# Performance work log

Hardware: AMD Instinct MI355X
Metric: run time of the kernel (lower is better)

## Reference

```python
import jax, jax.numpy as jnp
import numpy as np


def setup_inputs() -> dict:
    key = jax.random.key(0)
    ks = jax.random.split(key, 12)
    B, L, N, C, Ct, H, RH1, RH2, S = 64, 64, 256, 8, 4, 128, 128, 64, 4
    def rn(k, shape, s=0.08):
        return jax.random.normal(k, shape, dtype=jnp.float32) * s
    return dict(
        x=jax.random.normal(ks[0], (B, L, N, C * Ct), dtype=jnp.float32),
        hidden_intensity=jax.random.normal(ks[1], (B, N, H), dtype=jnp.float32),
        r=jax.random.normal(ks[2], (B, S), dtype=jnp.float32),
        W_ih=rn(ks[3], (4 * H, C)), W_hh=rn(ks[4], (4 * H, H)),
        b_ih=jnp.zeros((4 * H,), jnp.float32), b_hh=jnp.zeros((4 * H,), jnp.float32),
        W1=rn(ks[5], (RH1, 2 * H + 1)), b1=jnp.zeros((RH1,), jnp.float32),
        W2=rn(ks[6], (RH2, RH1)), b2=jnp.zeros((RH2,), jnp.float32),
        W3=rn(ks[7], (C, RH2)), b3=jnp.zeros((C,), jnp.float32),
        Wf=rn(ks[8], (1, C)), bf=jnp.zeros((1,), jnp.float32),
    )


def reference(x, hidden_intensity, r, W_ih, W_hh, b_ih, b_hh,
              W1, b1, W2, b2, W3, b3, Wf, bf):
    # Faithful to torch: nn.LSTM has batch_first=False but is fed (B, L, C),
    # so B is the sequence axis, L the batch axis, and lstm_out[:, -1, :]
    # writes predictions into that last column, so only x[:, -1] matters.
    B, L, N, _ = x.shape
    C = W_ih.shape[1]
    Ct = x.shape[3] // C
    H = W_hh.shape[1]

    def lstm_all_times(seq):  # seq: (T, Bb, C) -> hidden at every time (T, Bb, H)
        xp = jnp.einsum('tbc,gc->tbg', seq, W_ih) + b_ih + b_hh  # (T, Bb, 4H)
        def step(carry, xt):
            h, c = carry
            g = xt + h @ W_hh.T
            i, f, gg, o = jnp.split(g, 4, axis=-1)  # torch gate order i,f,g,o
            c = jax.nn.sigmoid(f) * c + jax.nn.sigmoid(i) * jnp.tanh(gg)
            h = jax.nn.sigmoid(o) * jnp.tanh(c)
            return (h, c), h
        z0 = jnp.zeros((seq.shape[1], H), seq.dtype)
        _, hs = jax.lax.scan(step, (z0, z0), xp)
        return hs

    hi = jnp.broadcast_to(hidden_intensity[:, :, None, :], (B, N, Ct, H))

    def roll(last_col, rj):  # last_col: (B, N, Ct, C), rj: (B,)
        hs = lstm_all_times(last_col.reshape(B, N * Ct, C)).reshape(B, N, Ct, H)
        rr = jnp.broadcast_to(rj[:, None, None, None], (B, N, Ct, 1))
        z = jnp.concatenate([hs, hi, rr], axis=-1)       # (B, N, Ct, 2H+1)
        h1 = jax.nn.relu(z @ W1.T + b1)
        h2 = jax.nn.relu(h1 @ W2.T + b2)
        pr = h2 @ W3.T + b3                              # (B, N, Ct, C)
        contrib = (jax.nn.relu(pr) @ Wf.T + bf)[..., 0].sum(axis=2)  # (B, N)
        return pr, contrib

    last0 = x[:, -1, :, :].reshape(B, N, Ct, C)
    _, preds = jax.lax.scan(roll, last0, r.T)  # (S, B, N)
    return jnp.transpose(preds, (1, 2, 0))     # (B, N, steps_ahead)
```

## Files before the change

### kernel.cpp

```cpp
#include <hip/hip_runtime.h>
#include <hip/hip_bf16.h>


typedef __attribute__((ext_vector_type(8))) _Float16 half8;
typedef __attribute__((ext_vector_type(4))) float f32x4;

#define MFMAH(a, b, c) __builtin_amdgcn_mfma_f32_16x16x32_f16(a, b, c, 0, 0, 0)

__device__ __forceinline__ float sigf(float x)   { return 1.0f / (1.0f + __expf(-x)); }
__device__ __forceinline__ float tanh_f(float x) { return 1.0f - 2.0f / (__expf(2.0f * x) + 1.0f); }

__global__ void prep_k(const float* __restrict__ x, const float* __restrict__ hi,
                       const float* __restrict__ W1, const float* __restrict__ W2,
                       const float* __restrict__ W3, const float* __restrict__ W_hh,
                       const float* __restrict__ W_ih,
                       _Float16* __restrict__ cur16, _Float16* __restrict__ hi16,
                       _Float16* __restrict__ wp1, _Float16* __restrict__ wp2,
                       _Float16* __restrict__ wp3, _Float16* __restrict__ wpB)
{
    int i = blockIdx.x * 256 + threadIdx.x;
    if (i < 65536) {
        int e = i * 8;
        int b = e >> 13, rem = e & 8191;
        const float* src = x + (size_t)b * 524288 + 63 * 8192 + rem;
        half8 v;
#pragma unroll
        for (int k = 0; k < 8; ++k) v[k] = (_Float16)src[k];
        *(half8*)(cur16 + e) = v;
        return;
    }
    i -= 65536;
    if (i < 262144) {
        int e = i * 8;
        half8 v;
#pragma unroll
        for (int k = 0; k < 8; ++k) v[k] = (_Float16)hi[e + k];
        *(half8*)(hi16 + e) = v;
        return;
    }
    i -= 262144;
    if (i < 32768) {
        int fragid = i >> 9, lj = i & 511;
        int kt = fragid >> 3, nt = fragid & 7;
        int l = lj >> 3, j = lj & 7;
        int k = kt * 32 + (l >> 4) * 8 + j;
        int o = nt * 16 + (l & 15);
        wp1[i] = (_Float16)W1[o * 257 + k];
        return;
    }
    i -= 32768;
    if (i < 8192) {
        int fragid = i >> 9, lj = i & 511;
        int kt = fragid >> 2, nt = fragid & 3;
        int l = lj >> 3, j = lj & 7;
        int k = kt * 32 + (l >> 4) * 8 + j;
        int o = nt * 16 + (l & 15);
        wp2[i] = (_Float16)W2[o * 128 + k];
        return;
    }
    i -= 8192;
    if (i < 1024) {
        int kt = i >> 9, lj = i & 511;
        int l = lj >> 3, j = lj & 7;
        int k = kt * 32 + (l >> 4) * 8 + j;
        int c = l & 15;
        wp3[i] = (_Float16)((c < 8) ? W3[c * 64 + k] : 0.0f);
        return;
    }
    i -= 1024;
    if (i < 81920) {
        int frag = i >> 9, lj = i & 511;
        int kt = frag >> 5, ntile = frag & 31;
        int l = lj >> 3, j = lj & 7;
        int klocal = (l >> 4) * 8 + j;
        int col = ntile * 16 + (l & 15);
        float v;
        if (kt < 4) v = W_hh[col * 128 + kt * 32 + klocal];
        else        v = (klocal < 8) ? W_ih[col * 8 + klocal] : 0.0f;
        wpB[i] = (_Float16)v;
    }
}

__global__ __launch_bounds__(512, 2) void lstm_mfma_k(
    const _Float16* __restrict__ cur16, const _Float16* __restrict__ wpB,
    const float* __restrict__ b_ih, const float* __restrict__ b_hh,
    _Float16* __restrict__ hs16)
{
    __shared__ __align__(16) _Float16 zone[2][4][640];
    __shared__ __align__(16) _Float16 xz[64][32];

    const int t  = threadIdx.x;
    const int cg = t >> 6, l = t & 63;
    const int li = l & 15, lk = l >> 4;
    const int q0 = blockIdx.x * 4;

    const int gsrc[4] = {1, 0, 2, 3};
    half8 bw[4][5];
#pragma unroll
    for (int g = 0; g < 4; ++g)
#pragma unroll
        for (int kt = 0; kt < 5; ++kt) {
            bw[g][kt] = *(const half8*)(wpB + (size_t)(kt * 32 + gsrc[g] * 8 + cg) * 512 + l * 8);
            asm volatile("" : "+a"(bw[g][kt]));
        }

    f32x4 bs4[4];
#pragma unroll
    for (int g = 0; g < 4; ++g) {
        int gc = gsrc[g] * 128 + cg * 16 + li;
        float bv = b_ih[gc] + b_hh[gc];
        bs4[g] = (f32x4){bv, bv, bv, bv};
    }

    for (int i = t; i < 1280; i += 512) ((uint*)zone)[i] = 0;
    if (t < 256) {
        int step = t >> 2, tt = t & 3;
        *(uint4*)&xz[step][tt * 8] =
            *(const uint4*)(cur16 + (size_t)step * 8192 + q0 * 8 + tt * 8);
    }
    float cc = 0.0f;
    __syncthreads();

    const int zpl   = cg >> 1;
    const int jl    = (cg & 1) * 16 + li;
    const int roff  = (li & 12) * 40 + lk * 8;
    const int srow  = lk * 4;

    _Float16* ph = hs16 + (size_t)(q0 + lk) * 128 + cg * 16 + li;
    const _Float16* xrd = &xz[0][(li >> 2) * 8];

    f32x4 accx[4];
    {
        half8 xa0 = *(const half8*)(xrd);
#pragma unroll
        for (int g = 0; g < 4; ++g)
            accx[g] = MFMAH(xa0, bw[g][4], bs4[g]);
    }

    auto dostep = [&](int step, int p) {
        const int pn = p ^ 1;

        half8 ah[4];
#pragma unroll
        for (int kt = 0; kt < 4; ++kt)
            ah[kt] = *(const half8*)&zone[p][kt][roff];

        __builtin_amdgcn_s_setprio(1);
        const f32x4 z4 = (f32x4){0.0f, 0.0f, 0.0f, 0.0f};
        f32x4 a0[4], a1[4];
#pragma unroll
        for (int g = 0; g < 4; ++g) {
            a0[g] = MFMAH(ah[0], bw[g][0], accx[g]);
            a1[g] = MFMAH(ah[2], bw[g][2], z4);
        }
#pragma unroll
        for (int g = 0; g < 4; ++g) {
            a0[g] = MFMAH(ah[1], bw[g][1], a0[g]);
            a1[g] = MFMAH(ah[3], bw[g][3], a1[g]);
        }

        float pf = a0[0][0] + a1[0][0];
        float sf = sigf(pf);
        float pi = a0[1][0] + a1[1][0];
        float pg = a0[2][0] + a1[2][0];
        float po = a0[3][0] + a1[3][0];
        cc = sf * cc + sigf(pi) * tanh_f(pg);
        float hv = sigf(po) * tanh_f(cc);
        __builtin_amdgcn_s_setprio(0);
        _Float16 h16 = (_Float16)hv;
        zone[pn][zpl][srow * 40 + jl] = h16;
        ph[(size_t)step * 131072] = h16;
        asm volatile("s_waitcnt lgkmcnt(0)\n\ts_barrier" ::: "memory");

        half8 xn = *(const half8*)(xrd + ((step + 1) & 63) * 32);
#pragma unroll
        for (int g = 0; g < 4; ++g)
            accx[g] = MFMAH(xn, bw[g][4], bs4[g]);
    };

    for (int s2 = 0; s2 < 32; ++s2) {
        dostep(s2 * 2,     0);
        dostep(s2 * 2 + 1, 1);
    }
}

__global__ __launch_bounds__(256, 3) void mlp_mfma_k(
    const _Float16* __restrict__ hs16, const _Float16* __restrict__ hi16,
    const float* __restrict__ r, int jstep,
    const _Float16* __restrict__ wp1, const _Float16* __restrict__ wp2,
    const _Float16* __restrict__ wp3,
    const float* __restrict__ W1, const float* __restrict__ b1,
    const float* __restrict__ b2, const float* __restrict__ b3,
    const float* __restrict__ Wf, const float* __restrict__ bfp,
    _Float16* __restrict__ cur16, float* __restrict__ out)
{
    __shared__ __align__(16) _Float16 h1f[4 * 4 * 640];
    __shared__ __align__(16) _Float16 h2f[2 * 4 * 640];

    const int t = threadIdx.x;
    const int w = t >> 6, l = t & 63;
    const int lrow = l & 15, lk = l >> 4;
    const int b = blockIdx.x >> 4;
    const int qb = (blockIdx.x & 15) * 64;
    const float rb = r[b * 4 + jstep];

    f32x4 acc[4][2];
#pragma unroll
    for (int nt = 0; nt < 2; ++nt) {
        int col = w * 32 + nt * 16 + lrow;
        float bias = b1[col] + rb * W1[col * 257 + 256];
#pragma unroll
        for (int mt = 0; mt < 4; ++mt)
            acc[mt][nt] = (f32x4){bias, bias, bias, bias};
    }

    auto loadA = [&](int kt, half8* av) {
#pragma unroll
        for (int mt = 0; mt < 4; ++mt) {
            int q = qb + mt * 16 + lrow;
            if (kt < 4)
                av[mt] = *(const half8*)(hs16 + (size_t)(b * 1024 + q) * 128
                                          + kt * 32 + lk * 8);
            else
                av[mt] = *(const half8*)(hi16 + (size_t)(b * 256 + (q >> 2)) * 128
                                          + (kt - 4) * 32 + lk * 8);
        }
    };

    half8 avA[4], avB[4];
    loadA(0, avA);
#pragma unroll
    for (int kt = 0; kt < 8; ++kt) {
        half8* cur = (kt & 1) ? avB : avA;
        half8* nxt = (kt & 1) ? avA : avB;
        if (kt < 7) loadA(kt + 1, nxt);
#pragma unroll
        for (int nt = 0; nt < 2; ++nt) {
            half8 bv = *(const half8*)(wp1 + (size_t)(kt * 8 + w * 2 + nt) * 512 + l * 8);
#pragma unroll
            for (int mt = 0; mt < 4; ++mt)
                acc[mt][nt] = MFMAH(cur[mt], bv, acc[mt][nt]);
        }
    }

#pragma unroll
    for (int mt = 0; mt < 4; ++mt)
#pragma unroll
        for (int nt = 0; nt < 2; ++nt)
#pragma unroll
            for (int reg = 0; reg < 4; ++reg) {
                float v = fmaxf(acc[mt][nt][reg], 0.0f);
                int s = lk * 4 + reg, jj = nt * 16 + lrow;
                h1f[(w * 4 + mt) * 640 + s * 40 + jj] = (_Float16)v;
            }
    __syncthreads();

    f32x4 acc2[4];
    {
        float bias = b2[16 * w + lrow];
#pragma unroll
        for (int mt = 0; mt < 4; ++mt)
            acc2[mt] = (f32x4){bias, bias, bias, bias};
    }
#pragma unroll
    for (int kt = 0; kt < 4; ++kt) {
        half8 bv = *(const half8*)(wp2 + (size_t)(kt * 4 + w) * 512 + l * 8);
#pragma unroll
        for (int mt = 0; mt < 4; ++mt) {
            half8 a = *(const half8*)&h1f[(kt * 4 + mt) * 640 + lrow * 40 + lk * 8];
            acc2[mt] = MFMAH(a, bv, acc2[mt]);
        }
    }
#pragma unroll
    for (int mt = 0; mt < 4; ++mt)
#pragma unroll
        for (int reg = 0; reg < 4; ++reg) {
            float v = fmaxf(acc2[mt][reg], 0.0f);
            int s = lk * 4 + reg, jl2 = (w & 1) * 16 + lrow;
            h2f[((w >> 1) * 4 + mt) * 640 + s * 40 + jl2] = (_Float16)v;
        }
    __syncthreads();

    f32x4 acc3 = (f32x4){0.0f, 0.0f, 0.0f, 0.0f};
#pragma unroll
    for (int kt = 0; kt < 2; ++kt) {
        half8 a  = *(const half8*)&h2f[(kt * 4 + w) * 640 + lrow * 40 + lk * 8];
        half8 bv = *(const half8*)(wp3 + (size_t)kt * 512 + l * 8);
        acc3 = MFMAH(a, bv, acc3);
    }

    const int c = lrow;
    const float b3v = (c < 8) ? b3[c] : 0.0f;
    const float wfv = (c < 8) ? Wf[c] : 0.0f;
    float fr[4];
#pragma unroll
    for (int reg = 0; reg < 4; ++reg) {
        float pr = acc3[reg] + b3v;
        if (c < 8) {
            int row = 16 * w + lk * 4 + reg;
            cur16[((size_t)(b * 1024 + qb + row)) * 8 + c] = (_Float16)pr;
        }
        fr[reg] = (c < 8) ? fmaxf(pr, 0.0f) * wfv : 0.0f;
    }
#pragma unroll
    for (int reg = 0; reg < 4; ++reg) {
        fr[reg] += __shfl_xor(fr[reg], 1);
        fr[reg] += __shfl_xor(fr[reg], 2);
        fr[reg] += __shfl_xor(fr[reg], 4);
    }
    if ((l & 15) == 0) {
        int n = (qb + 16 * w + lk * 4) >> 2;
        float v = fr[0] + fr[1] + fr[2] + fr[3] + 4.0f * bfp[0];
        out[(size_t)(b * 256 + n) * 4 + jstep] = v;
    }
}

extern "C" void kernel_launch(void* const* d_in, const int* in_sizes, int n_in,
                              void* d_out, int out_size, void* d_ws, size_t ws_size,
                              hipStream_t stream)
{
    const float* x   = (const float*)d_in[0];
    const float* hi  = (const float*)d_in[1];
    const float* r   = (const float*)d_in[2];
    const float* Wih = (const float*)d_in[3];
    const float* Whh = (const float*)d_in[4];
    const float* bih = (const float*)d_in[5];
    const float* bhh = (const float*)d_in[6];
    const float* W1  = (const float*)d_in[7];
    const float* b1  = (const float*)d_in[8];
    const float* W2  = (const float*)d_in[9];
    const float* b2  = (const float*)d_in[10];
    const float* W3  = (const float*)d_in[11];
    const float* b3  = (const float*)d_in[12];
    const float* Wf  = (const float*)d_in[13];
    const float* bf  = (const float*)d_in[14];
    float* out = (float*)d_out;

    _Float16* cur16 = (_Float16*)d_ws;
    _Float16* hs16  = cur16 + 524288;
    _Float16* hi16  = hs16 + 8388608;
    _Float16* wp1   = hi16 + 2097152;
    _Float16* wp2   = wp1 + 32768;
    _Float16* wp3   = wp2 + 8192;
    _Float16* wpB   = wp3 + 1024;

    prep_k<<<1764, 256, 0, stream>>>(x, hi, W1, W2, W3, Whh, Wih,
                                     cur16, hi16, wp1, wp2, wp3, wpB);
    for (int j = 0; j < 4; ++j) {
        lstm_mfma_k<<<256, 512, 0, stream>>>(cur16, wpB, bih, bhh, hs16);
        mlp_mfma_k<<<1024, 256, 0, stream>>>(hs16, hi16, r, j, wp1, wp2, wp3,
                                             W1, b1, b2, b3, Wf, bf, cur16, out);
    }
}
```

Measured before the change: 279.3 us.

## Split LSTM recurrence into 2-sequence blocks of 4 waves, 2 N-tiles per wave

```diff
diff --git a/kernel.cpp b/kernel.cpp
--- a/kernel.cpp
+++ b/kernel.cpp
@@ -81,101 +81,94 @@
     }
 }
 
-__global__ __launch_bounds__(512, 2) void lstm_mfma_k(
+__global__ __launch_bounds__(256, 2) void lstm_mfma_k(
     const _Float16* __restrict__ cur16, const _Float16* __restrict__ wpB,
     const float* __restrict__ b_ih, const float* __restrict__ b_hh,
     _Float16* __restrict__ hs16)
 {
-    __shared__ __align__(16) _Float16 zone[2][4][640];
-    __shared__ __align__(16) _Float16 xz[64][32];
+    __shared__ __align__(16) _Float16 zone[2][4][2][40];
+    __shared__ __align__(16) _Float16 xz[64][16];
 
     const int t  = threadIdx.x;
     const int cg = t >> 6, l = t & 63;
     const int li = l & 15, lk = l >> 4;
-    const int q0 = blockIdx.x * 4;
+    const int q0 = blockIdx.x * 2;
 
     const int gsrc[4] = {1, 0, 2, 3};
-    half8 bw[4][5];
+    half8 bw[4][2][5];
 #pragma unroll
     for (int g = 0; g < 4; ++g)
 #pragma unroll
-        for (int kt = 0; kt < 5; ++kt) {
-            bw[g][kt] = *(const half8*)(wpB + (size_t)(kt * 32 + gsrc[g] * 8 + cg) * 512 + l * 8);
-            asm volatile("" : "+a"(bw[g][kt]));
-        }
-
-    f32x4 bs4[4];
-#pragma unroll
-    for (int g = 0; g < 4; ++g) {
-        int gc = gsrc[g] * 128 + cg * 16 + li;
-        float bv = b_ih[gc] + b_hh[gc];
-        bs4[g] = (f32x4){bv, bv, bv, bv};
-    }
-
-    for (int i = t; i < 1280; i += 512) ((uint*)zone)[i] = 0;
-    if (t < 256) {
-        int step = t >> 2, tt = t & 3;
-        *(uint4*)&xz[step][tt * 8] =
-            *(const uint4*)(cur16 + (size_t)step * 8192 + q0 * 8 + tt * 8);
-    }
-    float cc = 0.0f;
+        for (int nt = 0; nt < 2; ++nt)
+#pragma unroll
+            for (int kt = 0; kt < 5; ++kt) {
+                bw[g][nt][kt] = *(const half8*)(wpB +
+                    (size_t)(kt * 32 + gsrc[g] * 8 + 2 * cg + nt) * 512 + l * 8);
+                asm volatile("" : "+a"(bw[g][nt][kt]));
+            }
+
+    float bias[4][2];
+#pragma unroll
+    for (int g = 0; g < 4; ++g)
+#pragma unroll
+        for (int nt = 0; nt < 2; ++nt) {
+            int gc = gsrc[g] * 128 + (2 * cg + nt) * 16 + li;
+            bias[g][nt] = b_ih[gc] + b_hh[gc];
+        }
+
+    if (t < 320) ((uint*)zone)[t] = 0;
+    if (t < 128) {
+        int step = t >> 1, s = t & 1;
+        *(uint4*)&xz[step][s * 8] =
+            *(const uint4*)(cur16 + (size_t)step * 8192 + (q0 + s) * 8);
+    }
+    float cc0 = 0.0f, cc1 = 0.0f;
     __syncthreads();
 
-    const int zpl   = cg >> 1;
-    const int jl    = (cg & 1) * 16 + li;
-    const int roff  = (li & 12) * 40 + lk * 8;
-    const int srow  = lk * 4;
-
-    _Float16* ph = hs16 + (size_t)(q0 + lk) * 128 + cg * 16 + li;
-    const _Float16* xrd = &xz[0][(li >> 2) * 8];
-
-    f32x4 accx[4];
-    {
-        half8 xa0 = *(const half8*)(xrd);
-#pragma unroll
-        for (int g = 0; g < 4; ++g)
-            accx[g] = MFMAH(xa0, bw[g][4], bs4[g]);
-    }
+    const int sli  = (li >> 2) & 1;
+    const int roff = sli * 40 + lk * 8;
+    const _Float16* xrd = &xz[0][sli * 8];
+
+    _Float16* ph = hs16 + (size_t)(q0 + lk) * 128 + cg * 32 + li;
+
+    const f32x4 z4 = (f32x4){0.0f, 0.0f, 0.0f, 0.0f};
 
     auto dostep = [&](int step, int p) {
         const int pn = p ^ 1;
-
+        half8 xa = *(const half8*)(xrd + step * 16);
         half8 ah[4];
 #pragma unroll
         for (int kt = 0; kt < 4; ++kt)
-            ah[kt] = *(const half8*)&zone[p][kt][roff];
+            ah[kt] = *(const half8*)&zone[p][kt][0][roff];
 
         __builtin_amdgcn_s_setprio(1);
-        const f32x4 z4 = (f32x4){0.0f, 0.0f, 0.0f, 0.0f};
-        f32x4 a0[4], a1[4];
+        float pv[4][2];
 #pragma unroll
         for (int g = 0; g < 4; ++g) {
-            a0[g] = MFMAH(ah[0], bw[g][0], accx[g]);
-            a1[g] = MFMAH(ah[2], bw[g][2], z4);
-        }
-#pragma unroll
-        for (int g = 0; g < 4; ++g) {
-            a0[g] = MFMAH(ah[1], bw[g][1], a0[g]);
-            a1[g] = MFMAH(ah[3], bw[g][3], a1[g]);
-        }
-
-        float pf = a0[0][0] + a1[0][0];
-        float sf = sigf(pf);
-        float pi = a0[1][0] + a1[1][0];
-        float pg = a0[2][0] + a1[2][0];
-        float po = a0[3][0] + a1[3][0];
-        cc = sf * cc + sigf(pi) * tanh_f(pg);
-        float hv = sigf(po) * tanh_f(cc);
+            f32x4 a0 = MFMAH(xa, bw[g][0][4], z4);
+            f32x4 a1 = MFMAH(xa, bw[g][1][4], z4);
+#pragma unroll
+            for (int kt = 0; kt < 4; ++kt) {
+                a0 = MFMAH(ah[kt], bw[g][0][kt], a0);
+                a1 = MFMAH(ah[kt], bw[g][1][kt], a1);
+            }
+            pv[g][0] = a0[0] + bias[g][0];
+            pv[g][1] = a1[0] + bias[g][1];
+        }
+
+        cc0 = sigf(pv[0][0]) * cc0 + sigf(pv[1][0]) * tanh_f(pv[2][0]);
+        float hv0 = sigf(pv[3][0]) * tanh_f(cc0);
+        cc1 = sigf(pv[0][1]) * cc1 + sigf(pv[1][1]) * tanh_f(pv[2][1]);
+        float hv1 = sigf(pv[3][1]) * tanh_f(cc1);
         __builtin_amdgcn_s_setprio(0);
-        _Float16 h16 = (_Float16)hv;
-        zone[pn][zpl][srow * 40 + jl] = h16;
-        ph[(size_t)step * 131072] = h16;
+        _Float16 h0 = (_Float16)hv0, h1 = (_Float16)hv1;
+        if (lk < 2) {
+            zone[pn][cg][lk][li]      = h0;
+            zone[pn][cg][lk][16 + li] = h1;
+            ph[(size_t)step * 131072]      = h0;
+            ph[(size_t)step * 131072 + 16] = h1;
+        }
         asm volatile("s_waitcnt lgkmcnt(0)\n\ts_barrier" ::: "memory");
-
-        half8 xn = *(const half8*)(xrd + ((step + 1) & 63) * 32);
-#pragma unroll
-        for (int g = 0; g < 4; ++g)
-            accx[g] = MFMAH(xn, bw[g][4], bs4[g]);
     };
 
     for (int s2 = 0; s2 < 32; ++s2) {
@@ -347,7 +340,7 @@
     prep_k<<<1764, 256, 0, stream>>>(x, hi, W1, W2, W3, Whh, Wih,
                                      cur16, hi16, wp1, wp2, wp3, wpB);
     for (int j = 0; j < 4; ++j) {
-        lstm_mfma_k<<<256, 512, 0, stream>>>(cur16, wpB, bih, bhh, hs16);
+        lstm_mfma_k<<<512, 256, 0, stream>>>(cur16, wpB, bih, bhh, hs16);
         mlp_mfma_k<<<1024, 256, 0, stream>>>(hs16, hi16, r, j, wp1, wp2, wp3,
                                              W1, b1, b2, b3, Wf, bf, cur16, out);
     }
```

Result: slower. 396.7 us (+42.0%).

## Fuse LSTM and MLP across all rollout steps into one persistent kernel

Applied to the files above, without the earlier changes.

```diff
diff --git a/kernel.cpp b/kernel.cpp
--- a/kernel.cpp
+++ b/kernel.cpp
@@ -10,26 +10,15 @@
 __device__ __forceinline__ float sigf(float x)   { return 1.0f / (1.0f + __expf(-x)); }
 __device__ __forceinline__ float tanh_f(float x) { return 1.0f - 2.0f / (__expf(2.0f * x) + 1.0f); }
 
-__global__ void prep_k(const float* __restrict__ x, const float* __restrict__ hi,
+__global__ void prep_k(const float* __restrict__ hi,
                        const float* __restrict__ W1, const float* __restrict__ W2,
                        const float* __restrict__ W3, const float* __restrict__ W_hh,
                        const float* __restrict__ W_ih,
-                       _Float16* __restrict__ cur16, _Float16* __restrict__ hi16,
-                       _Float16* __restrict__ wp1, _Float16* __restrict__ wp2,
-                       _Float16* __restrict__ wp3, _Float16* __restrict__ wpB)
+                       _Float16* __restrict__ hi16, _Float16* __restrict__ wp1,
+                       _Float16* __restrict__ wp2, _Float16* __restrict__ wp3,
+                       _Float16* __restrict__ wpB)
 {
     int i = blockIdx.x * 256 + threadIdx.x;
-    if (i < 65536) {
-        int e = i * 8;
-        int b = e >> 13, rem = e & 8191;
-        const float* src = x + (size_t)b * 524288 + 63 * 8192 + rem;
-        half8 v;
-#pragma unroll
-        for (int k = 0; k < 8; ++k) v[k] = (_Float16)src[k];
-        *(half8*)(cur16 + e) = v;
-        return;
-    }
-    i -= 65536;
     if (i < 262144) {
         int e = i * 8;
         half8 v;
@@ -39,16 +28,19 @@
         return;
     }
     i -= 262144;
-    if (i < 32768) {
+    if (i < 36864) {
         int fragid = i >> 9, lj = i & 511;
         int kt = fragid >> 3, nt = fragid & 7;
         int l = lj >> 3, j = lj & 7;
-        int k = kt * 32 + (l >> 4) * 8 + j;
+        int klocal = (l >> 4) * 8 + j;
         int o = nt * 16 + (l & 15);
-        wp1[i] = (_Float16)W1[o * 257 + k];
+        float v;
+        if (kt < 8)      v = W1[o * 257 + kt * 32 + klocal];
+        else             v = (klocal == 0) ? W1[o * 257 + 256] : 0.0f;
+        wp1[i] = (_Float16)v;
         return;
     }
-    i -= 32768;
+    i -= 36864;
     if (i < 8192) {
         int fragid = i >> 9, lj = i & 511;
         int kt = fragid >> 2, nt = fragid & 3;
@@ -81,18 +73,26 @@
     }
 }
 
-__global__ __launch_bounds__(512, 2) void lstm_mfma_k(
-    const _Float16* __restrict__ cur16, const _Float16* __restrict__ wpB,
+__global__ __launch_bounds__(512, 2) void fused_k(
+    const float* __restrict__ x, const _Float16* __restrict__ hi16,
+    const float* __restrict__ r, const _Float16* __restrict__ wpB,
     const float* __restrict__ b_ih, const float* __restrict__ b_hh,
-    _Float16* __restrict__ hs16)
+    const _Float16* __restrict__ wp1, const _Float16* __restrict__ wp2,
+    const _Float16* __restrict__ wp3, const float* __restrict__ b1,
+    const float* __restrict__ b2, const float* __restrict__ b3,
+    const float* __restrict__ Wf, const float* __restrict__ bfp,
+    float* __restrict__ out)
 {
     __shared__ __align__(16) _Float16 zone[2][4][640];
     __shared__ __align__(16) _Float16 xz[64][32];
+    __shared__ __align__(16) _Float16 hsL[256 * 130];
+    __shared__ __align__(16) _Float16 h1L[128 * 132];
+    __shared__ __align__(16) _Float16 h2L[128 * 68];
 
     const int t  = threadIdx.x;
     const int cg = t >> 6, l = t & 63;
     const int li = l & 15, lk = l >> 4;
-    const int q0 = blockIdx.x * 4;
+    const int q0 = blockIdx.x * 4, nblk = blockIdx.x;
 
     const int gsrc[4] = {1, 0, 2, 3};
     half8 bw[4][5];
@@ -103,7 +103,6 @@
             bw[g][kt] = *(const half8*)(wpB + (size_t)(kt * 32 + gsrc[g] * 8 + cg) * 512 + l * 8);
             asm volatile("" : "+a"(bw[g][kt]));
         }
-
     f32x4 bs4[4];
 #pragma unroll
     for (int g = 0; g < 4; ++g) {
@@ -112,206 +111,176 @@
         bs4[g] = (f32x4){bv, bv, bv, bv};
     }
 
-    for (int i = t; i < 1280; i += 512) ((uint*)zone)[i] = 0;
     if (t < 256) {
         int step = t >> 2, tt = t & 3;
-        *(uint4*)&xz[step][tt * 8] =
-            *(const uint4*)(cur16 + (size_t)step * 8192 + q0 * 8 + tt * 8);
-    }
-    float cc = 0.0f;
-    __syncthreads();
-
-    const int zpl   = cg >> 1;
-    const int jl    = (cg & 1) * 16 + li;
-    const int roff  = (li & 12) * 40 + lk * 8;
-    const int srow  = lk * 4;
-
-    _Float16* ph = hs16 + (size_t)(q0 + lk) * 128 + cg * 16 + li;
+        const float* src = x + (size_t)step * 524288 + 63 * 8192 + (q0 + tt) * 8;
+        half8 v;
+#pragma unroll
+        for (int k = 0; k < 8; ++k) v[k] = (_Float16)src[k];
+        *(half8*)&xz[step][tt * 8] = v;
+    }
+
+    const int zpl  = cg >> 1;
+    const int jl   = (cg & 1) * 16 + li;
+    const int roff = (li & 12) * 40 + lk * 8;
+    const int srow = lk * 4;
     const _Float16* xrd = &xz[0][(li >> 2) * 8];
-
-    f32x4 accx[4];
-    {
-        half8 xa0 = *(const half8*)(xrd);
-#pragma unroll
-        for (int g = 0; g < 4; ++g)
-            accx[g] = MFMAH(xa0, bw[g][4], bs4[g]);
-    }
-
-    auto dostep = [&](int step, int p) {
-        const int pn = p ^ 1;
-
-        half8 ah[4];
-#pragma unroll
-        for (int kt = 0; kt < 4; ++kt)
-            ah[kt] = *(const half8*)&zone[p][kt][roff];
-
-        __builtin_amdgcn_s_setprio(1);
-        const f32x4 z4 = (f32x4){0.0f, 0.0f, 0.0f, 0.0f};
-        f32x4 a0[4], a1[4];
-#pragma unroll
-        for (int g = 0; g < 4; ++g) {
-            a0[g] = MFMAH(ah[0], bw[g][0], accx[g]);
-            a1[g] = MFMAH(ah[2], bw[g][2], z4);
+    const f32x4 z4 = (f32x4){0.0f, 0.0f, 0.0f, 0.0f};
+
+    for (int j = 0; j < 4; ++j) {
+        for (int i = t; i < 1280; i += 512) ((uint*)zone)[i] = 0;
+        float cc = 0.0f;
+        __syncthreads();
+
+        f32x4 accx[4];
+        {
+            half8 xa0 = *(const half8*)(xrd);
+#pragma unroll
+            for (int g = 0; g < 4; ++g)
+                accx[g] = MFMAH(xa0, bw[g][4], bs4[g]);
         }
-#pragma unroll
-        for (int g = 0; g < 4; ++g) {
-            a0[g] = MFMAH(ah[1], bw[g][1], a0[g]);
-            a1[g] = MFMAH(ah[3], bw[g][3], a1[g]);
+
+        auto dostep = [&](int step, int p) {
+            const int pn = p ^ 1;
+            half8 ah[4];
+#pragma unroll
+            for (int kt = 0; kt < 4; ++kt)
+                ah[kt] = *(const half8*)&zone[p][kt][roff];
+
+            __builtin_amdgcn_s_setprio(1);
+            f32x4 a0[4], a1[4];
+#pragma unroll
+            for (int g = 0; g < 4; ++g) {
+                a0[g] = MFMAH(ah[0], bw[g][0], accx[g]);
+                a1[g] = MFMAH(ah[2], bw[g][2], z4);
+            }
+#pragma unroll
+            for (int g = 0; g < 4; ++g) {
+                a0[g] = MFMAH(ah[1], bw[g][1], a0[g]);
+                a1[g] = MFMAH(ah[3], bw[g][3], a1[g]);
+            }
+            float pf = a0[0][0] + a1[0][0];
+            float sf = sigf(pf);
+            float pi = a0[1][0] + a1[1][0];
+            float pg = a0[2][0] + a1[2][0];
+            float po = a0[3][0] + a1[3][0];
+            cc = sf * cc + sigf(pi) * tanh_f(pg);
+            float hv = sigf(po) * tanh_f(cc);
+            __builtin_amdgcn_s_setprio(0);
+            _Float16 h16 = (_Float16)hv;
+            zone[pn][zpl][srow * 40 + jl] = h16;
+            hsL[(step * 4 + lk) * 130 + cg * 16 + li] = h16;
+            asm volatile("s_waitcnt lgkmcnt(0)\n\ts_barrier" ::: "memory");
+
+            half8 xn = *(const half8*)(xrd + ((step + 1) & 63) * 32);
+#pragma unroll
+            for (int g = 0; g < 4; ++g)
+                accx[g] = MFMAH(xn, bw[g][4], bs4[g]);
+        };
+        for (int s2 = 0; s2 < 32; ++s2) {
+            dostep(s2 * 2,     0);
+            dostep(s2 * 2 + 1, 1);
         }
 
-        float pf = a0[0][0] + a1[0][0];
-        float sf = sigf(pf);
-        float pi = a0[1][0] + a1[1][0];
-        float pg = a0[2][0] + a1[2][0];
-        float po = a0[3][0] + a1[3][0];
-        cc = sf * cc + sigf(pi) * tanh_f(pg);
-        float hv = sigf(po) * tanh_f(cc);
-        __builtin_amdgcn_s_setprio(0);
-        _Float16 h16 = (_Float16)hv;
-        zone[pn][zpl][srow * 40 + jl] = h16;
-        ph[(size_t)step * 131072] = h16;
-        asm volatile("s_waitcnt lgkmcnt(0)\n\ts_barrier" ::: "memory");
-
-        half8 xn = *(const half8*)(xrd + ((step + 1) & 63) * 32);
-#pragma unroll
-        for (int g = 0; g < 4; ++g)
-            accx[g] = MFMAH(xn, bw[g][4], bs4[g]);
-    };
-
-    for (int s2 = 0; s2 < 32; ++s2) {
-        dostep(s2 * 2,     0);
-        dostep(s2 * 2 + 1, 1);
-    }
-}
-
-__global__ __launch_bounds__(256, 3) void mlp_mfma_k(
-    const _Float16* __restrict__ hs16, const _Float16* __restrict__ hi16,
-    const float* __restrict__ r, int jstep,
-    const _Float16* __restrict__ wp1, const _Float16* __restrict__ wp2,
-    const _Float16* __restrict__ wp3,
-    const float* __restrict__ W1, const float* __restrict__ b1,
-    const float* __restrict__ b2, const float* __restrict__ b3,
-    const float* __restrict__ Wf, const float* __restrict__ bfp,
-    _Float16* __restrict__ cur16, float* __restrict__ out)
-{
-    __shared__ __align__(16) _Float16 h1f[4 * 4 * 640];
-    __shared__ __align__(16) _Float16 h2f[2 * 4 * 640];
-
-    const int t = threadIdx.x;
-    const int w = t >> 6, l = t & 63;
-    const int lrow = l & 15, lk = l >> 4;
-    const int b = blockIdx.x >> 4;
-    const int qb = (blockIdx.x & 15) * 64;
-    const float rb = r[b * 4 + jstep];
-
-    f32x4 acc[4][2];
-#pragma unroll
-    for (int nt = 0; nt < 2; ++nt) {
-        int col = w * 32 + nt * 16 + lrow;
-        float bias = b1[col] + rb * W1[col * 257 + 256];
-#pragma unroll
-        for (int mt = 0; mt < 4; ++mt)
-            acc[mt][nt] = (f32x4){bias, bias, bias, bias};
-    }
-
-    auto loadA = [&](int kt, half8* av) {
-#pragma unroll
-        for (int mt = 0; mt < 4; ++mt) {
-            int q = qb + mt * 16 + lrow;
-            if (kt < 4)
-                av[mt] = *(const half8*)(hs16 + (size_t)(b * 1024 + q) * 128
-                                          + kt * 32 + lk * 8);
-            else
-                av[mt] = *(const half8*)(hi16 + (size_t)(b * 256 + (q >> 2)) * 128
-                                          + (kt - 4) * 32 + lk * 8);
+#pragma unroll 1
+        for (int p = 0; p < 2; ++p) {
+            f32x4 acc[8];
+            {
+                float bias = b1[cg * 16 + li];
+#pragma unroll
+                for (int m = 0; m < 8; ++m)
+                    acc[m] = (f32x4){bias, bias, bias, bias};
+            }
+#pragma unroll
+            for (int kt = 0; kt < 9; ++kt) {
+                half8 bv = *(const half8*)(wp1 + (size_t)(kt * 8 + cg) * 512 + l * 8);
+#pragma unroll
+                for (int m = 0; m < 8; ++m) {
+                    int Mg = p * 8 + m;
+                    half8 av;
+                    if (kt < 4) {
+                        av = *(const half8*)&hsL[(Mg * 16 + li) * 130 + kt * 32 + lk * 8];
+                    } else if (kt < 8) {
+                        int b = Mg * 4 + (li >> 2);
+                        av = *(const half8*)(hi16 + ((size_t)b * 256 + nblk) * 128
+                                             + (kt - 4) * 32 + lk * 8);
+                    } else {
+                        int b = Mg * 4 + (li >> 2);
+                        av = (half8){0, 0, 0, 0, 0, 0, 0, 0};
+                        if (lk == 0) av[0] = (_Float16)r[b * 4 + j];
+                    }
+                    acc[m] = MFMAH(av, bv, acc[m]);
+                }
+            }
+#pragma unroll
+            for (int m = 0; m < 8; ++m)
+#pragma unroll
+                for (int reg = 0; reg < 4; ++reg) {
+                    float v = fmaxf(acc[m][reg], 0.0f);
+                    h1L[(m * 16 + lk * 4 + reg) * 132 + cg * 16 + li] = (_Float16)v;
+                }
+            __syncthreads();
+
+            {
+                const int n2 = cg & 3, mg0 = (cg >> 2) * 4;
+                f32x4 acc2[4];
+                float bias = b2[n2 * 16 + li];
+#pragma unroll
+                for (int mi = 0; mi < 4; ++mi)
+                    acc2[mi] = (f32x4){bias, bias, bias, bias};
+#pragma unroll
+                for (int kt = 0; kt < 4; ++kt) {
+                    half8 bv = *(const half8*)(wp2 + (size_t)(kt * 4 + n2) * 512 + l * 8);
+#pragma unroll
+                    for (int mi = 0; mi < 4; ++mi) {
+                        int m = mg0 + mi;
+                        half8 av = *(const half8*)&h1L[(m * 16 + li) * 132 + kt * 32 + lk * 8];
+                        acc2[mi] = MFMAH(av, bv, acc2[mi]);
+                    }
+                }
+#pragma unroll
+                for (int mi = 0; mi < 4; ++mi)
+#pragma unroll
+                    for (int reg = 0; reg < 4; ++reg) {
+                        float v = fmaxf(acc2[mi][reg], 0.0f);
+                        h2L[((mg0 + mi) * 16 + lk * 4 + reg) * 68 + n2 * 16 + li] = (_Float16)v;
+                    }
+            }
+            __syncthreads();
+
+            {
+                f32x4 acc3 = z4;
+#pragma unroll
+                for (int kt = 0; kt < 2; ++kt) {
+                    half8 av = *(const half8*)&h2L[(cg * 16 + li) * 68 + kt * 32 + lk * 8];
+                    half8 bv = *(const half8*)(wp3 + (size_t)kt * 512 + l * 8);
+                    acc3 = MFMAH(av, bv, acc3);
+                }
+                const int Mg = p * 8 + cg;
+                const int c = li;
+                const float b3v = (c < 8) ? b3[c] : 0.0f;
+                const float wfv = (c < 8) ? Wf[c] : 0.0f;
+                const int b = Mg * 4 + lk;
+                float fr[4];
+#pragma unroll
+                for (int reg = 0; reg < 4; ++reg) {
+                    float pr = acc3[reg] + b3v;
+                    if (c < 8) xz[b][reg * 8 + c] = (_Float16)pr;
+                    fr[reg] = (c < 8) ? fmaxf(pr, 0.0f) * wfv : 0.0f;
+                }
+#pragma unroll
+                for (int reg = 0; reg < 4; ++reg) {
+                    fr[reg] += __shfl_xor(fr[reg], 1);
+                    fr[reg] += __shfl_xor(fr[reg], 2);
+                    fr[reg] += __shfl_xor(fr[reg], 4);
+                }
+                if (li == 0) {
+                    float v = fr[0] + fr[1] + fr[2] + fr[3] + 4.0f * bfp[0];
+                    out[((size_t)b * 256 + nblk) * 4 + j] = v;
+                }
+            }
+            __syncthreads();
         }
-    };
-
-    half8 avA[4], avB[4];
-    loadA(0, avA);
-#pragma unroll
-    for (int kt = 0; kt < 8; ++kt) {
-        half8* cur = (kt & 1) ? avB : avA;
-        half8* nxt = (kt & 1) ? avA : avB;
-        if (kt < 7) loadA(kt + 1, nxt);
-#pragma unroll
-        for (int nt = 0; nt < 2; ++nt) {
-            half8 bv = *(const half8*)(wp1 + (size_t)(kt * 8 + w * 2 + nt) * 512 + l * 8);
-#pragma unroll
-            for (int mt = 0; mt < 4; ++mt)
-                acc[mt][nt] = MFMAH(cur[mt], bv, acc[mt][nt]);
-        }
-    }
-
-#pragma unroll
-    for (int mt = 0; mt < 4; ++mt)
-#pragma unroll
-        for (int nt = 0; nt < 2; ++nt)
-#pragma unroll
-            for (int reg = 0; reg < 4; ++reg) {
-                float v = fmaxf(acc[mt][nt][reg], 0.0f);
-                int s = lk * 4 + reg, jj = nt * 16 + lrow;
-                h1f[(w * 4 + mt) * 640 + s * 40 + jj] = (_Float16)v;
-            }
-    __syncthreads();
-
-    f32x4 acc2[4];
-    {
-        float bias = b2[16 * w + lrow];
-#pragma unroll
-        for (int mt = 0; mt < 4; ++mt)
-            acc2[mt] = (f32x4){bias, bias, bias, bias};
-    }
-#pragma unroll
-    for (int kt = 0; kt < 4; ++kt) {
-        half8 bv = *(const half8*)(wp2 + (size_t)(kt * 4 + w) * 512 + l * 8);
-#pragma unroll
-        for (int mt = 0; mt < 4; ++mt) {
-            half8 a = *(const half8*)&h1f[(kt * 4 + mt) * 640 + lrow * 40 + lk * 8];
-            acc2[mt] = MFMAH(a, bv, acc2[mt]);
-        }
-    }
-#pragma unroll
-    for (int mt = 0; mt < 4; ++mt)
-#pragma unroll
-        for (int reg = 0; reg < 4; ++reg) {
-            float v = fmaxf(acc2[mt][reg], 0.0f);
-            int s = lk * 4 + reg, jl2 = (w & 1) * 16 + lrow;
-            h2f[((w >> 1) * 4 + mt) * 640 + s * 40 + jl2] = (_Float16)v;
-        }
-    __syncthreads();
-
-    f32x4 acc3 = (f32x4){0.0f, 0.0f, 0.0f, 0.0f};
-#pragma unroll
-    for (int kt = 0; kt < 2; ++kt) {
-        half8 a  = *(const half8*)&h2f[(kt * 4 + w) * 640 + lrow * 40 + lk * 8];
-        half8 bv = *(const half8*)(wp3 + (size_t)kt * 512 + l * 8);
-        acc3 = MFMAH(a, bv, acc3);
-    }
-
-    const int c = lrow;
-    const float b3v = (c < 8) ? b3[c] : 0.0f;
-    const float wfv = (c < 8) ? Wf[c] : 0.0f;
-    float fr[4];
-#pragma unroll
-    for (int reg = 0; reg < 4; ++reg) {
-        float pr = acc3[reg] + b3v;
-        if (c < 8) {
-            int row = 16 * w + lk * 4 + reg;
-            cur16[((size_t)(b * 1024 + qb + row)) * 8 + c] = (_Float16)pr;
-        }
-        fr[reg] = (c < 8) ? fmaxf(pr, 0.0f) * wfv : 0.0f;
-    }
-#pragma unroll
-    for (int reg = 0; reg < 4; ++reg) {
-        fr[reg] += __shfl_xor(fr[reg], 1);
-        fr[reg] += __shfl_xor(fr[reg], 2);
-        fr[reg] += __shfl_xor(fr[reg], 4);
-    }
-    if ((l & 15) == 0) {
-        int n = (qb + 16 * w + lk * 4) >> 2;
-        float v = fr[0] + fr[1] + fr[2] + fr[3] + 4.0f * bfp[0];
-        out[(size_t)(b * 256 + n) * 4 + jstep] = v;
     }
 }
 
@@ -336,19 +305,14 @@
     const float* bf  = (const float*)d_in[14];
     float* out = (float*)d_out;
 
-    _Float16* cur16 = (_Float16*)d_ws;
-    _Float16* hs16  = cur16 + 524288;
-    _Float16* hi16  = hs16 + 8388608;
-    _Float16* wp1   = hi16 + 2097152;
-    _Float16* wp2   = wp1 + 32768;
-    _Float16* wp3   = wp2 + 8192;
-    _Float16* wpB   = wp3 + 1024;
-
-    prep_k<<<1764, 256, 0, stream>>>(x, hi, W1, W2, W3, Whh, Wih,
-                                     cur16, hi16, wp1, wp2, wp3, wpB);
-    for (int j = 0; j < 4; ++j) {
-        lstm_mfma_k<<<256, 512, 0, stream>>>(cur16, wpB, bih, bhh, hs16);
-        mlp_mfma_k<<<1024, 256, 0, stream>>>(hs16, hi16, r, j, wp1, wp2, wp3,
-                                             W1, b1, b2, b3, Wf, bf, cur16, out);
-    }
+    _Float16* hi16 = (_Float16*)d_ws;
+    _Float16* wp1  = hi16 + 2097152;
+    _Float16* wp2  = wp1 + 36864;
+    _Float16* wp3  = wp2 + 8192;
+    _Float16* wpB  = wp3 + 1024;
+
+    prep_k<<<1524, 256, 0, stream>>>(hi, W1, W2, W3, Whh, Wih,
+                                     hi16, wp1, wp2, wp3, wpB);
+    fused_k<<<256, 512, 0, stream>>>(x, hi16, r, wpB, bih, bhh,
+                                     wp1, wp2, wp3, b1, b2, b3, Wf, bf, out);
 }
```

Measured after the change: 281.3 us. No clear change (+0.7%).
